# Kernel optimization log

Hardware: AMD Instinct MI355X
Metric: run time of the kernel (lower is better)

## Reference

```python
import jax, jax.numpy as jnp
import numpy as np

EPS = 0.001          # sinkhorn_args['eps']
MAX_ITERS = 100      # sinkhorn_args['max_iters'] (torch early-stops at a fixed point;
                     # running all iters yields the same converged values within tol)


def setup_inputs() -> dict:
    key = jax.random.key(0)
    B, N, d_in, n_ref = 64, 2048, 128, 256
    X = jax.random.normal(key, (B, N, d_in), dtype=jnp.float32)
    # uniform_ref = linspace(-1,1,n_ref) repeated across d_in (the learned parameter's init)
    reference = jnp.tile(jnp.linspace(-1.0, 1.0, n_ref, dtype=jnp.float32)[:, None], (1, d_in))
    return {"X": X, "reference": reference}


def _cdist(a, b):
    # Euclidean pairwise distance (p=2) via gram trick; avoids B x n x m x d blowup.
    a2 = jnp.sum(a * a, axis=-1)[:, :, None]   # (B, n, 1)
    b2 = jnp.sum(b * b, axis=-1)[:, None, :]   # (B, 1, m)
    sq = a2 + b2 - 2.0 * jnp.einsum("bnd,bmd->bnm", a, b)
    return jnp.sqrt(jnp.maximum(sq, 0.0))


def reference(X, reference):
    B, N, d = X.shape
    n_ref = reference.shape[0]
    ref_b = jnp.broadcast_to(reference[None], (B, n_ref, d))
    C = _cdist(ref_b, X)                       # (B, n_ref, N)
    # uniform weights -> scalar log-weights
    log_wx = jnp.log(1.0 / n_ref + 1e-8)
    log_wy = jnp.log(1.0 / N + 1e-8)

    def step(carry, _):
        u, v = carry
        u = EPS * (log_wx - jax.nn.logsumexp((-C + v[:, None, :]) / EPS, axis=2))
        v = EPS * (log_wy - jax.nn.logsumexp((-C + u[:, :, None]) / EPS, axis=1))
        return (u, v), None

    u0 = jnp.zeros((B, n_ref), dtype=C.dtype)
    v0 = jnp.zeros((B, N), dtype=C.dtype)
    (u, v), _ = jax.lax.scan(step, (u0, v0), None, length=MAX_ITERS)

    P = jnp.exp((-C + u[:, :, None] + v[:, None, :]) / EPS)   # transport plan (B, n_ref, N)
    denom = jnp.sum(P, axis=2, keepdims=True) + 1e-8
    barycenters = jnp.einsum("bnm,bmd->bnd", P, X) / denom
    return barycenters - reference[None]       # (B, n_ref, d_in)
```

## Files before the change

kernel.cpp:

```cpp
#include <hip/hip_runtime.h>
#include <math.h>

#define BATCH 64
#define NREF  256
#define NPTS  2048
#define DIM   128
#define ITERS 100
#define INV_EPS 1000.0f
#define RCHUNK 16
#define NCHUNK (NREF / RCHUNK)


__global__ __launch_bounds__(256) void r2_kernel(const float* __restrict__ ref,
                                                 float* __restrict__ r2) {
    int i = threadIdx.x;
    const float4* r4 = (const float4*)(ref + (size_t)i * DIM);
    float acc = 0.f;
#pragma unroll
    for (int k = 0; k < DIM / 4; ++k) {
        float4 a = r4[k];
        acc += a.x * a.x + a.y * a.y + a.z * a.z + a.w * a.w;
    }
    r2[i] = acc;
}

__global__ __launch_bounds__(256) void x2_kernel(const float* __restrict__ X,
                                                 float* __restrict__ x2) {
    int r = threadIdx.x >> 4;
    int c = threadIdx.x & 15;
    int j = blockIdx.x * 16 + r;
    const float4* xp = (const float4*)(X + (size_t)j * DIM + c * 8);
    float4 a = xp[0], b = xp[1];
    float acc = a.x * a.x + a.y * a.y + a.z * a.z + a.w * a.w
              + b.x * b.x + b.y * b.y + b.z * b.z + b.w * b.w;
#pragma unroll
    for (int off = 1; off < 16; off <<= 1) acc += __shfl_xor(acc, off);
    if (c == 0) x2[j] = acc;
}

__global__ __launch_bounds__(256) void cgemm_kernel(const float* __restrict__ X,
                                                    const float* __restrict__ ref,
                                                    const float* __restrict__ r2,
                                                    const float* __restrict__ x2,
                                                    float* __restrict__ C) {
    __shared__ float rs[8 * 128];
    __shared__ float xs[8 * 128];
    int b  = blockIdx.x >> 5;
    int it = (blockIdx.x >> 4) & 1;
    int jt = blockIdx.x & 15;
    int i0 = it * 128, j0 = jt * 128;
    int t  = threadIdx.x;
    int ti = t >> 4, tj = t & 15;

    int sr = t >> 1;
    int sh = (t & 1) * 4;
    const float* refp = ref + (size_t)(i0 + sr) * DIM + sh;
    const float* xp   = X + ((size_t)b * NPTS + j0 + sr) * DIM + sh;

    float4 acc[2][2][4];
#pragma unroll
    for (int p = 0; p < 2; ++p)
#pragma unroll
        for (int q = 0; q < 2; ++q)
#pragma unroll
            for (int ii = 0; ii < 4; ++ii)
                acc[p][q][ii] = make_float4(0.f, 0.f, 0.f, 0.f);

    for (int k0 = 0; k0 < DIM; k0 += 8) {
        float4 rv = *(const float4*)(refp + k0);
        float4 xv = *(const float4*)(xp + k0);
        __syncthreads();
        rs[(sh + 0) * 128 + sr] = rv.x; rs[(sh + 1) * 128 + sr] = rv.y;
        rs[(sh + 2) * 128 + sr] = rv.z; rs[(sh + 3) * 128 + sr] = rv.w;
        xs[(sh + 0) * 128 + sr] = xv.x; xs[(sh + 1) * 128 + sr] = xv.y;
        xs[(sh + 2) * 128 + sr] = xv.z; xs[(sh + 3) * 128 + sr] = xv.w;
        __syncthreads();

        const float4* rs4 = (const float4*)rs;
        const float4* xs4 = (const float4*)xs;
#pragma unroll
        for (int k = 0; k < 8; ++k) {
            float4 a0 = rs4[k * 32 + ti];
            float4 a1 = rs4[k * 32 + 16 + ti];
            float4 b0 = xs4[k * 32 + tj];
            float4 b1 = xs4[k * 32 + 16 + tj];
#define FMA4(ACC, S, BV)                                                     \
            ACC.x = fmaf(S, BV.x, ACC.x); ACC.y = fmaf(S, BV.y, ACC.y);      \
            ACC.z = fmaf(S, BV.z, ACC.z); ACC.w = fmaf(S, BV.w, ACC.w);
#define ROW(P, S, II)                                                        \
            FMA4(acc[P][0][II], S, b0) FMA4(acc[P][1][II], S, b1)
            ROW(0, a0.x, 0) ROW(0, a0.y, 1) ROW(0, a0.z, 2) ROW(0, a0.w, 3)
            ROW(1, a1.x, 0) ROW(1, a1.y, 1) ROW(1, a1.z, 2) ROW(1, a1.w, 3)
#undef ROW
#undef FMA4
        }
    }

    float4 x2v[2];
    x2v[0] = *(const float4*)(x2 + (size_t)b * NPTS + j0 + tj * 4);
    x2v[1] = *(const float4*)(x2 + (size_t)b * NPTS + j0 + 64 + tj * 4);
#pragma unroll
    for (int p = 0; p < 2; ++p)
#pragma unroll
        for (int ii = 0; ii < 4; ++ii) {
            int i = i0 + p * 64 + ti * 4 + ii;
            float rr = r2[i];
            float* crow = C + ((size_t)b * NREF + i) * NPTS + j0;
#pragma unroll
            for (int q = 0; q < 2; ++q) {
                float4 av = acc[p][q][ii];
                float4 o;
                o.x = sqrtf(fmaxf(rr + x2v[q].x - 2.f * av.x, 0.f)) * INV_EPS;
                o.y = sqrtf(fmaxf(rr + x2v[q].y - 2.f * av.y, 0.f)) * INV_EPS;
                o.z = sqrtf(fmaxf(rr + x2v[q].z - 2.f * av.z, 0.f)) * INV_EPS;
                o.w = sqrtf(fmaxf(rr + x2v[q].w - 2.f * av.w, 0.f)) * INV_EPS;
                *(float4*)(crow + q * 64 + tj * 4) = o;
            }
        }
}

__global__ __launch_bounds__(512, 4) void uv_kernel(const float* __restrict__ C,
                                                    const float* __restrict__ v,
                                                    float* __restrict__ u,
                                                    float* __restrict__ Pl,
                                                    float log_wx) {
    __shared__ float smx[RCHUNK][8];
    __shared__ float sms[RCHUNK][8];
    int b     = blockIdx.x >> 4;
    int chunk = blockIdx.x & 15;
    int t     = threadIdx.x;
    int lane  = t & 63;
    int w     = t >> 6;

    const float* Cb = C + (size_t)(b * NREF + chunk * RCHUNK) * NPTS;
    float4 vj = *(const float4*)(v + (size_t)b * NPTS + 4 * t);

    float4 a[RCHUNK];
#pragma unroll
    for (int i = 0; i < RCHUNK; ++i)
        a[i] = *(const float4*)(Cb + (size_t)i * NPTS + 4 * t);

    float m[RCHUNK], su[RCHUNK];
#pragma unroll
    for (int i = 0; i < RCHUNK; ++i) {
        a[i].x = vj.x - a[i].x; a[i].y = vj.y - a[i].y;
        a[i].z = vj.z - a[i].z; a[i].w = vj.w - a[i].w;
        m[i] = fmaxf(fmaxf(a[i].x, a[i].y), fmaxf(a[i].z, a[i].w));
    }
#pragma unroll
    for (int i = 0; i < RCHUNK; ++i)
#pragma unroll
        for (int off = 1; off < 64; off <<= 1)
            m[i] = fmaxf(m[i], __shfl_xor(m[i], off));
    if (lane == 0) {
#pragma unroll
        for (int i = 0; i < RCHUNK; ++i) smx[i][w] = m[i];
    }
    __syncthreads();
#pragma unroll
    for (int i = 0; i < RCHUNK; ++i) {
        float mm = smx[i][0];
#pragma unroll
        for (int q = 1; q < 8; ++q) mm = fmaxf(mm, smx[i][q]);
        m[i] = mm;
    }
#pragma unroll
    for (int i = 0; i < RCHUNK; ++i)
        su[i] = __expf(a[i].x - m[i]) + __expf(a[i].y - m[i])
              + __expf(a[i].z - m[i]) + __expf(a[i].w - m[i]);
#pragma unroll
    for (int i = 0; i < RCHUNK; ++i)
#pragma unroll
        for (int off = 1; off < 64; off <<= 1)
            su[i] += __shfl_xor(su[i], off);
    if (lane == 0) {
#pragma unroll
        for (int i = 0; i < RCHUNK; ++i) sms[i][w] = su[i];
    }
    __syncthreads();
#pragma unroll
    for (int i = 0; i < RCHUNK; ++i) {
        float s = ((sms[i][0] + sms[i][1]) + (sms[i][2] + sms[i][3]))
                + ((sms[i][4] + sms[i][5]) + (sms[i][6] + sms[i][7]));
        su[i] = log_wx - (m[i] + __logf(s));
    }
    int ub = b * NREF + chunk * RCHUNK;
#pragma unroll
    for (int i = 0; i < RCHUNK; ++i)
        if (t == i) u[ub + i] = su[i];

    float4 pl;
#define COLL(Q)                                                              \
    {                                                                        \
        float mq = a[0].Q + su[0];                                           \
        _Pragma("unroll")                                                    \
        for (int i_ = 1; i_ < RCHUNK; ++i_)                                  \
            mq = fmaxf(mq, a[i_].Q + su[i_]);                                \
        float sq_ = 0.f;                                                     \
        _Pragma("unroll")                                                    \
        for (int i_ = 0; i_ < RCHUNK; ++i_)                                  \
            sq_ += __expf(a[i_].Q + su[i_] - mq);                            \
        pl.Q = (mq - vj.Q) + __logf(sq_);                                    \
    }
    COLL(x) COLL(y) COLL(z) COLL(w)
#undef COLL
    *(float4*)(Pl + (size_t)(b * NCHUNK + chunk) * NPTS + 4 * t) = pl;
}

__global__ __launch_bounds__(256) void vmerge_kernel(const float* __restrict__ Pl,
                                                     float* __restrict__ v,
                                                     float log_wy) {
    int b = blockIdx.x >> 3;
    int j = ((blockIdx.x & 7) << 8) + threadIdx.x;
    const float* p = Pl + (size_t)b * NCHUNK * NPTS + j;
    float l[NCHUNK];
#pragma unroll
    for (int c = 0; c < NCHUNK; ++c) l[c] = p[(size_t)c * NPTS];
    float m = l[0];
#pragma unroll
    for (int c = 1; c < NCHUNK; ++c) m = fmaxf(m, l[c]);
    float s = 0.f;
#pragma unroll
    for (int c = 0; c < NCHUNK; ++c) s += __expf(l[c] - m);
    v[(size_t)b * NPTS + j] = log_wy - (m + __logf(s));
}

__global__ __launch_bounds__(256) void out_kernel(const float* __restrict__ C,
                                                  const float* __restrict__ X,
                                                  const float* __restrict__ ref,
                                                  const float* __restrict__ u,
                                                  const float* __restrict__ v,
                                                  float* __restrict__ out) {
    __shared__ float wt[32 * 32];
    __shared__ float xt[32 * DIM];
    int b  = blockIdx.x >> 3;
    int it = blockIdx.x & 7;
    int i0 = it * 32;
    int t  = threadIdx.x;
    int s  = t & 31;
    int g  = t >> 5;

    const float* Cb = C + ((size_t)b * NREF + i0) * NPTS;
    const float* vb = v + (size_t)b * NPTS;
    const float* ub = u + (size_t)b * NREF + i0;

    float4 acc[4];
    float wsum[4];
#pragma unroll
    for (int r = 0; r < 4; ++r) { acc[r] = make_float4(0.f, 0.f, 0.f, 0.f); wsum[r] = 0.f; }

    for (int j0 = 0; j0 < NPTS; j0 += 32) {
#pragma unroll
        for (int k = 0; k < 4; ++k) {
            int widx = t + 256 * k;
            int r    = widx >> 5;
            int jj   = widx & 31;
            wt[widx] = __expf(ub[r] + vb[j0 + jj] - Cb[(size_t)r * NPTS + j0 + jj]);
        }
        const float4* Xb4 = (const float4*)(X + ((size_t)b * NPTS + j0) * DIM);
#pragma unroll
        for (int k = 0; k < 4; ++k) {
            int idx = t + 256 * k;
            ((float4*)xt)[idx] = Xb4[idx];
        }
        __syncthreads();

        const float4* xt4 = (const float4*)xt;
#pragma unroll 2
        for (int jj = 0; jj < 32; jj += 4) {
            float4 xv0 = xt4[(jj + 0) * 32 + s];
            float4 xv1 = xt4[(jj + 1) * 32 + s];
            float4 xv2 = xt4[(jj + 2) * 32 + s];
            float4 xv3 = xt4[(jj + 3) * 32 + s];
#pragma unroll
            for (int r = 0; r < 4; ++r) {
                float4 w4 = *(const float4*)&wt[(g * 4 + r) * 32 + jj];
                acc[r].x = fmaf(w4.x, xv0.x, acc[r].x); acc[r].y = fmaf(w4.x, xv0.y, acc[r].y);
                acc[r].z = fmaf(w4.x, xv0.z, acc[r].z); acc[r].w = fmaf(w4.x, xv0.w, acc[r].w);
                acc[r].x = fmaf(w4.y, xv1.x, acc[r].x); acc[r].y = fmaf(w4.y, xv1.y, acc[r].y);
                acc[r].z = fmaf(w4.y, xv1.z, acc[r].z); acc[r].w = fmaf(w4.y, xv1.w, acc[r].w);
                acc[r].x = fmaf(w4.z, xv2.x, acc[r].x); acc[r].y = fmaf(w4.z, xv2.y, acc[r].y);
                acc[r].z = fmaf(w4.z, xv2.z, acc[r].z); acc[r].w = fmaf(w4.z, xv2.w, acc[r].w);
                acc[r].x = fmaf(w4.w, xv3.x, acc[r].x); acc[r].y = fmaf(w4.w, xv3.y, acc[r].y);
                acc[r].z = fmaf(w4.w, xv3.z, acc[r].z); acc[r].w = fmaf(w4.w, xv3.w, acc[r].w);
                wsum[r] += (w4.x + w4.y) + (w4.z + w4.w);
            }
        }
        __syncthreads();
    }

#pragma unroll
    for (int r = 0; r < 4; ++r) {
        int i = i0 + g * 4 + r;
        float dn = wsum[r] + 1e-8f;
        float inv = 1.0f / dn;
        float4 rf = ((const float4*)(ref + (size_t)i * DIM))[s];
        float4 o;
        o.x = acc[r].x * inv - rf.x;
        o.y = acc[r].y * inv - rf.y;
        o.z = acc[r].z * inv - rf.z;
        o.w = acc[r].w * inv - rf.w;
        ((float4*)(out + ((size_t)b * NREF + i) * DIM))[s] = o;
    }
}

extern "C" void kernel_launch(void* const* d_in, const int* in_sizes, int n_in,
                              void* d_out, int out_size, void* d_ws, size_t ws_size,
                              hipStream_t stream) {
    const float* X   = (const float*)d_in[0];
    const float* ref = (const float*)d_in[1];
    float* out = (float*)d_out;

    char* ws = (char*)d_ws;
    size_t o = 0;
    float* C  = (float*)(ws + o); o += (size_t)BATCH * NREF * NPTS * sizeof(float);
    float* u  = (float*)(ws + o); o += (size_t)BATCH * NREF * sizeof(float);
    float* v  = (float*)(ws + o); o += (size_t)BATCH * NPTS * sizeof(float);
    float* r2 = (float*)(ws + o); o += 4096;
    float* x2 = (float*)(ws + o); o += (size_t)BATCH * NPTS * sizeof(float);
    float* Pl = (float*)(ws + o); o += (size_t)BATCH * NCHUNK * NPTS * sizeof(float);

    const float log_wx = (float)log(1.0 / (double)NREF + 1e-8);
    const float log_wy = (float)log(1.0 / (double)NPTS + 1e-8);

    hipMemsetAsync(v, 0, (size_t)BATCH * NPTS * sizeof(float), stream);

    x2_kernel<<<BATCH * NPTS / 16, 256, 0, stream>>>(X, x2);
    r2_kernel<<<1, 256, 0, stream>>>(ref, r2);
    cgemm_kernel<<<BATCH * 32, 256, 0, stream>>>(X, ref, r2, x2, C);

    for (int t = 0; t < ITERS; ++t) {
        uv_kernel<<<BATCH * NCHUNK, 512, 0, stream>>>(C, v, u, Pl, log_wx);
        vmerge_kernel<<<BATCH * NPTS / 256, 256, 0, stream>>>(Pl, v, log_wy);
    }

    out_kernel<<<BATCH * 8, 256, 0, stream>>>(C, X, ref, u, v, out);
}
```

Measured before the change: 4.344 ms.

## Fold norm kernels into cgemm and split output GEMM over points with atomics

The row norms of ref and X are now accumulated inside the C GEMM from the tiles it already loads, which removes two small kernels and their launches. The output barycenter kernel is reorganised so each block covers all 256 reference rows over a 256-point slice of N, computing exp weights once per C element into swizzled shared memory. Each block adds its partial numerators and denominators into the reused Pl buffer with atomics, and a small finish kernel then divides and subtracts ref. This reduces repeated X reloads across row tiles, but adds atomic traffic, a memset and an extra launch.

```diff
diff --git a/kernel.cpp b/kernel.cpp
--- a/kernel.cpp
+++ b/kernel.cpp
@@ -11,40 +11,13 @@
 #define NCHUNK (NREF / RCHUNK)
 
 
-__global__ __launch_bounds__(256) void r2_kernel(const float* __restrict__ ref,
-                                                 float* __restrict__ r2) {
-    int i = threadIdx.x;
-    const float4* r4 = (const float4*)(ref + (size_t)i * DIM);
-    float acc = 0.f;
-#pragma unroll
-    for (int k = 0; k < DIM / 4; ++k) {
-        float4 a = r4[k];
-        acc += a.x * a.x + a.y * a.y + a.z * a.z + a.w * a.w;
-    }
-    r2[i] = acc;
-}
-
-__global__ __launch_bounds__(256) void x2_kernel(const float* __restrict__ X,
-                                                 float* __restrict__ x2) {
-    int r = threadIdx.x >> 4;
-    int c = threadIdx.x & 15;
-    int j = blockIdx.x * 16 + r;
-    const float4* xp = (const float4*)(X + (size_t)j * DIM + c * 8);
-    float4 a = xp[0], b = xp[1];
-    float acc = a.x * a.x + a.y * a.y + a.z * a.z + a.w * a.w
-              + b.x * b.x + b.y * b.y + b.z * b.z + b.w * b.w;
-#pragma unroll
-    for (int off = 1; off < 16; off <<= 1) acc += __shfl_xor(acc, off);
-    if (c == 0) x2[j] = acc;
-}
-
 __global__ __launch_bounds__(256) void cgemm_kernel(const float* __restrict__ X,
                                                     const float* __restrict__ ref,
-                                                    const float* __restrict__ r2,
-                                                    const float* __restrict__ x2,
                                                     float* __restrict__ C) {
     __shared__ float rs[8 * 128];
     __shared__ float xs[8 * 128];
+    __shared__ float r2s[128];
+    __shared__ float x2s[128];
     int b  = blockIdx.x >> 5;
     int it = (blockIdx.x >> 4) & 1;
     int jt = blockIdx.x & 15;
@@ -65,10 +38,13 @@
 #pragma unroll
             for (int ii = 0; ii < 4; ++ii)
                 acc[p][q][ii] = make_float4(0.f, 0.f, 0.f, 0.f);
+    float rsq = 0.f, xsq = 0.f;
 
     for (int k0 = 0; k0 < DIM; k0 += 8) {
         float4 rv = *(const float4*)(refp + k0);
         float4 xv = *(const float4*)(xp + k0);
+        rsq += rv.x * rv.x + rv.y * rv.y + rv.z * rv.z + rv.w * rv.w;
+        xsq += xv.x * xv.x + xv.y * xv.y + xv.z * xv.z + xv.w * xv.w;
         __syncthreads();
         rs[(sh + 0) * 128 + sr] = rv.x; rs[(sh + 1) * 128 + sr] = rv.y;
         rs[(sh + 2) * 128 + sr] = rv.z; rs[(sh + 3) * 128 + sr] = rv.w;
@@ -96,24 +72,33 @@
         }
     }
 
-    float4 x2v[2];
-    x2v[0] = *(const float4*)(x2 + (size_t)b * NPTS + j0 + tj * 4);
-    x2v[1] = *(const float4*)(x2 + (size_t)b * NPTS + j0 + 64 + tj * 4);
+    rsq += __shfl_xor(rsq, 1);
+    xsq += __shfl_xor(xsq, 1);
+    if ((t & 1) == 0) { r2s[sr] = rsq; x2s[sr] = xsq; }
+    __syncthreads();
+
+    float x2v[2][4];
+#pragma unroll
+    for (int q = 0; q < 2; ++q)
+#pragma unroll
+        for (int e = 0; e < 4; ++e)
+            x2v[q][e] = x2s[q * 64 + tj * 4 + e];
+
 #pragma unroll
     for (int p = 0; p < 2; ++p)
 #pragma unroll
         for (int ii = 0; ii < 4; ++ii) {
-            int i = i0 + p * 64 + ti * 4 + ii;
-            float rr = r2[i];
-            float* crow = C + ((size_t)b * NREF + i) * NPTS + j0;
+            int il = p * 64 + ti * 4 + ii;
+            float rr = r2s[il];
+            float* crow = C + ((size_t)b * NREF + i0 + il) * NPTS + j0;
 #pragma unroll
             for (int q = 0; q < 2; ++q) {
                 float4 av = acc[p][q][ii];
                 float4 o;
-                o.x = sqrtf(fmaxf(rr + x2v[q].x - 2.f * av.x, 0.f)) * INV_EPS;
-                o.y = sqrtf(fmaxf(rr + x2v[q].y - 2.f * av.y, 0.f)) * INV_EPS;
-                o.z = sqrtf(fmaxf(rr + x2v[q].z - 2.f * av.z, 0.f)) * INV_EPS;
-                o.w = sqrtf(fmaxf(rr + x2v[q].w - 2.f * av.w, 0.f)) * INV_EPS;
+                o.x = sqrtf(fmaxf(rr + x2v[q][0] - 2.f * av.x, 0.f)) * INV_EPS;
+                o.y = sqrtf(fmaxf(rr + x2v[q][1] - 2.f * av.y, 0.f)) * INV_EPS;
+                o.z = sqrtf(fmaxf(rr + x2v[q][2] - 2.f * av.z, 0.f)) * INV_EPS;
+                o.w = sqrtf(fmaxf(rr + x2v[q][3] - 2.f * av.w, 0.f)) * INV_EPS;
                 *(float4*)(crow + q * 64 + tj * 4) = o;
             }
         }
@@ -225,83 +210,126 @@
     v[(size_t)b * NPTS + j] = log_wy - (m + __logf(s));
 }
 
-__global__ __launch_bounds__(256) void out_kernel(const float* __restrict__ C,
-                                                  const float* __restrict__ X,
-                                                  const float* __restrict__ ref,
-                                                  const float* __restrict__ u,
-                                                  const float* __restrict__ v,
-                                                  float* __restrict__ out) {
-    __shared__ float wt[32 * 32];
+__global__ __launch_bounds__(512, 4) void out_partial(const float* __restrict__ C,
+                                                      const float* __restrict__ X,
+                                                      const float* __restrict__ u,
+                                                      const float* __restrict__ v,
+                                                      float* __restrict__ num,
+                                                      float* __restrict__ den) {
+    __shared__ float wts[NREF * 32];
     __shared__ float xt[32 * DIM];
     int b  = blockIdx.x >> 3;
-    int it = blockIdx.x & 7;
-    int i0 = it * 32;
+    int jc = blockIdx.x & 7;
+    int j0 = jc * 256;
     int t  = threadIdx.x;
-    int s  = t & 31;
-    int g  = t >> 5;
-
-    const float* Cb = C + ((size_t)b * NREF + i0) * NPTS;
-    const float* vb = v + (size_t)b * NPTS;
-    const float* ub = u + (size_t)b * NREF + i0;
-
-    float4 acc[4];
-    float wsum[4];
-#pragma unroll
-    for (int r = 0; r < 4; ++r) { acc[r] = make_float4(0.f, 0.f, 0.f, 0.f); wsum[r] = 0.f; }
-
-    for (int j0 = 0; j0 < NPTS; j0 += 32) {
+    int s  = t & 15;
+    int g  = t >> 4;
+
+    const float* Cb = C + (size_t)b * NREF * NPTS + j0;
+    const float* ub = u + b * NREF;
+    const float* vb = v + (size_t)b * NPTS + j0;
+
+    float4 a0[8], a1[8];
+    float ws[8];
+#pragma unroll
+    for (int r = 0; r < 8; ++r) {
+        a0[r] = make_float4(0.f, 0.f, 0.f, 0.f);
+        a1[r] = make_float4(0.f, 0.f, 0.f, 0.f);
+        ws[r] = 0.f;
+    }
+
+    for (int jt = 0; jt < 256; jt += 32) {
 #pragma unroll
         for (int k = 0; k < 4; ++k) {
-            int widx = t + 256 * k;
-            int r    = widx >> 5;
-            int jj   = widx & 31;
-            wt[widx] = __expf(ub[r] + vb[j0 + jj] - Cb[(size_t)r * NPTS + j0 + jj]);
+            int fidx = t + 512 * k;
+            int r = fidx >> 3, q = fidx & 7;
+            float4 cv = *(const float4*)(Cb + (size_t)r * NPTS + jt + 4 * q);
+            float4 vv = *(const float4*)(vb + jt + 4 * q);
+            float uu = ub[r];
+            float4 wv;
+            wv.x = __expf(uu + vv.x - cv.x);
+            wv.y = __expf(uu + vv.y - cv.y);
+            wv.z = __expf(uu + vv.z - cv.z);
+            wv.w = __expf(uu + vv.w - cv.w);
+            int sw = q ^ ((r >> 3) & 7);
+            *(float4*)&wts[r * 32 + sw * 4] = wv;
         }
-        const float4* Xb4 = (const float4*)(X + ((size_t)b * NPTS + j0) * DIM);
-#pragma unroll
-        for (int k = 0; k < 4; ++k) {
-            int idx = t + 256 * k;
-            ((float4*)xt)[idx] = Xb4[idx];
-        }
+        const float4* Xb4 = (const float4*)(X + ((size_t)b * NPTS + j0 + jt) * DIM);
+        ((float4*)xt)[t]       = Xb4[t];
+        ((float4*)xt)[t + 512] = Xb4[t + 512];
         __syncthreads();
 
         const float4* xt4 = (const float4*)xt;
-#pragma unroll 2
-        for (int jj = 0; jj < 32; jj += 4) {
-            float4 xv0 = xt4[(jj + 0) * 32 + s];
-            float4 xv1 = xt4[(jj + 1) * 32 + s];
-            float4 xv2 = xt4[(jj + 2) * 32 + s];
-            float4 xv3 = xt4[(jj + 3) * 32 + s];
-#pragma unroll
-            for (int r = 0; r < 4; ++r) {
-                float4 w4 = *(const float4*)&wt[(g * 4 + r) * 32 + jj];
-                acc[r].x = fmaf(w4.x, xv0.x, acc[r].x); acc[r].y = fmaf(w4.x, xv0.y, acc[r].y);
-                acc[r].z = fmaf(w4.x, xv0.z, acc[r].z); acc[r].w = fmaf(w4.x, xv0.w, acc[r].w);
-                acc[r].x = fmaf(w4.y, xv1.x, acc[r].x); acc[r].y = fmaf(w4.y, xv1.y, acc[r].y);
-                acc[r].z = fmaf(w4.y, xv1.z, acc[r].z); acc[r].w = fmaf(w4.y, xv1.w, acc[r].w);
-                acc[r].x = fmaf(w4.z, xv2.x, acc[r].x); acc[r].y = fmaf(w4.z, xv2.y, acc[r].y);
-                acc[r].z = fmaf(w4.z, xv2.z, acc[r].z); acc[r].w = fmaf(w4.z, xv2.w, acc[r].w);
-                acc[r].x = fmaf(w4.w, xv3.x, acc[r].x); acc[r].y = fmaf(w4.w, xv3.y, acc[r].y);
-                acc[r].z = fmaf(w4.w, xv3.z, acc[r].z); acc[r].w = fmaf(w4.w, xv3.w, acc[r].w);
-                wsum[r] += (w4.x + w4.y) + (w4.z + w4.w);
+#pragma unroll
+        for (int jp = 0; jp < 16; ++jp) {
+            int j1 = 2 * jp;
+            float4 xa0 = xt4[j1 * 32 + s];
+            float4 xa1 = xt4[j1 * 32 + 16 + s];
+            float4 xb0 = xt4[(j1 + 1) * 32 + s];
+            float4 xb1 = xt4[(j1 + 1) * 32 + 16 + s];
+            int q   = jp >> 1;
+            int h   = jp & 1;
+            int swb = (q ^ (g & 7)) * 4 + 2 * h;
+#pragma unroll
+            for (int rr = 0; rr < 8; ++rr) {
+                int r = g * 8 + rr;
+                float2 w2 = *(const float2*)&wts[r * 32 + swb];
+                a0[rr].x = fmaf(w2.x, xa0.x, a0[rr].x);
+                a0[rr].y = fmaf(w2.x, xa0.y, a0[rr].y);
+                a0[rr].z = fmaf(w2.x, xa0.z, a0[rr].z);
+                a0[rr].w = fmaf(w2.x, xa0.w, a0[rr].w);
+                a1[rr].x = fmaf(w2.x, xa1.x, a1[rr].x);
+                a1[rr].y = fmaf(w2.x, xa1.y, a1[rr].y);
+                a1[rr].z = fmaf(w2.x, xa1.z, a1[rr].z);
+                a1[rr].w = fmaf(w2.x, xa1.w, a1[rr].w);
+                a0[rr].x = fmaf(w2.y, xb0.x, a0[rr].x);
+                a0[rr].y = fmaf(w2.y, xb0.y, a0[rr].y);
+                a0[rr].z = fmaf(w2.y, xb0.z, a0[rr].z);
+                a0[rr].w = fmaf(w2.y, xb0.w, a0[rr].w);
+                a1[rr].x = fmaf(w2.y, xb1.x, a1[rr].x);
+                a1[rr].y = fmaf(w2.y, xb1.y, a1[rr].y);
+                a1[rr].z = fmaf(w2.y, xb1.z, a1[rr].z);
+                a1[rr].w = fmaf(w2.y, xb1.w, a1[rr].w);
+                ws[rr] += w2.x + w2.y;
             }
         }
         __syncthreads();
     }
 
 #pragma unroll
-    for (int r = 0; r < 4; ++r) {
-        int i = i0 + g * 4 + r;
-        float dn = wsum[r] + 1e-8f;
-        float inv = 1.0f / dn;
-        float4 rf = ((const float4*)(ref + (size_t)i * DIM))[s];
-        float4 o;
-        o.x = acc[r].x * inv - rf.x;
-        o.y = acc[r].y * inv - rf.y;
-        o.z = acc[r].z * inv - rf.z;
-        o.w = acc[r].w * inv - rf.w;
-        ((float4*)(out + ((size_t)b * NREF + i) * DIM))[s] = o;
-    }
+    for (int rr = 0; rr < 8; ++rr) {
+        int r = g * 8 + rr;
+        float* nrow = num + ((size_t)b * NREF + r) * DIM;
+        unsafeAtomicAdd(nrow + 4 * s + 0, a0[rr].x);
+        unsafeAtomicAdd(nrow + 4 * s + 1, a0[rr].y);
+        unsafeAtomicAdd(nrow + 4 * s + 2, a0[rr].z);
+        unsafeAtomicAdd(nrow + 4 * s + 3, a0[rr].w);
+        unsafeAtomicAdd(nrow + 64 + 4 * s + 0, a1[rr].x);
+        unsafeAtomicAdd(nrow + 64 + 4 * s + 1, a1[rr].y);
+        unsafeAtomicAdd(nrow + 64 + 4 * s + 2, a1[rr].z);
+        unsafeAtomicAdd(nrow + 64 + 4 * s + 3, a1[rr].w);
+        if (s == 0) unsafeAtomicAdd(den + b * NREF + r, ws[rr]);
+    }
+}
+
+__global__ __launch_bounds__(256) void out_finish(const float* __restrict__ num,
+                                                  const float* __restrict__ den,
+                                                  const float* __restrict__ ref,
+                                                  float* __restrict__ out) {
+    int fidx = blockIdx.x * 256 + threadIdx.x;
+    int b = fidx >> 13;
+    int w = fidx & 8191;
+    int i = w >> 5;
+    int q = w & 31;
+    float4 n4 = ((const float4*)num)[fidx];
+    float inv = 1.0f / (den[(b << 8) + i] + 1e-8f);
+    float4 rf = ((const float4*)ref)[i * 32 + q];
+    float4 o;
+    o.x = n4.x * inv - rf.x;
+    o.y = n4.y * inv - rf.y;
+    o.z = n4.z * inv - rf.z;
+    o.w = n4.w * inv - rf.w;
+    ((float4*)out)[fidx] = o;
 }
 
 extern "C" void kernel_launch(void* const* d_in, const int* in_sizes, int n_in,
@@ -313,26 +341,28 @@
 
     char* ws = (char*)d_ws;
     size_t o = 0;
-    float* C  = (float*)(ws + o); o += (size_t)BATCH * NREF * NPTS * sizeof(float);
-    float* u  = (float*)(ws + o); o += (size_t)BATCH * NREF * sizeof(float);
-    float* v  = (float*)(ws + o); o += (size_t)BATCH * NPTS * sizeof(float);
-    float* r2 = (float*)(ws + o); o += 4096;
-    float* x2 = (float*)(ws + o); o += (size_t)BATCH * NPTS * sizeof(float);
-    float* Pl = (float*)(ws + o); o += (size_t)BATCH * NCHUNK * NPTS * sizeof(float);
+    float* C   = (float*)(ws + o); o += (size_t)BATCH * NREF * NPTS * sizeof(float);
+    float* u   = (float*)(ws + o); o += (size_t)BATCH * NREF * sizeof(float);
+    float* v   = (float*)(ws + o); o += (size_t)BATCH * NPTS * sizeof(float);
+    float* Pl  = (float*)(ws + o); o += (size_t)BATCH * NCHUNK * NPTS * sizeof(float);
+    float* den = (float*)(ws + o); o += (size_t)BATCH * NREF * sizeof(float);
+    float* num = Pl;
 
     const float log_wx = (float)log(1.0 / (double)NREF + 1e-8);
     const float log_wy = (float)log(1.0 / (double)NPTS + 1e-8);
 
     hipMemsetAsync(v, 0, (size_t)BATCH * NPTS * sizeof(float), stream);
 
-    x2_kernel<<<BATCH * NPTS / 16, 256, 0, stream>>>(X, x2);
-    r2_kernel<<<1, 256, 0, stream>>>(ref, r2);
-    cgemm_kernel<<<BATCH * 32, 256, 0, stream>>>(X, ref, r2, x2, C);
+    cgemm_kernel<<<BATCH * 32, 256, 0, stream>>>(X, ref, C);
 
     for (int t = 0; t < ITERS; ++t) {
         uv_kernel<<<BATCH * NCHUNK, 512, 0, stream>>>(C, v, u, Pl, log_wx);
         vmerge_kernel<<<BATCH * NPTS / 256, 256, 0, stream>>>(Pl, v, log_wy);
     }
 
-    out_kernel<<<BATCH * 8, 256, 0, stream>>>(C, X, ref, u, v, out);
-}
+    hipMemsetAsync(num, 0,
+                   ((size_t)BATCH * NCHUNK * NPTS + (size_t)BATCH * NREF) * sizeof(float),
+                   stream);
+    out_partial<<<BATCH * 8, 512, 0, stream>>>(C, X, u, v, num, den);
+    out_finish<<<BATCH * NREF * DIM / 1024, 256, 0, stream>>>(num, den, ref, out);
+}
```

After: 6.392 ms. 1.47x slower.
